# Kernel optimization log

Measured on AMD Instinct MI355X. Metric: run time of the kernel, lower is better.

Reference implementation:

```python
import jax, jax.numpy as jnp
import numpy as np

B, T, D, H = 4, 2048, 1024, 16
HD = D // H  # head_dim = 64


def setup_inputs() -> dict:
    key = jax.random.key(0)
    k1, k2, k3 = jax.random.split(key, 3)
    x = jax.random.normal(k1, (B, T, D), dtype=jnp.float32)
    # torch Linear weights: [out_features, in_features], kaiming-ish scale
    Wqkv = jax.random.normal(k2, (3 * D, D), dtype=jnp.float32) * (1.0 / np.sqrt(D))
    Wout = jax.random.normal(k3, (D, D), dtype=jnp.float32) * (1.0 / np.sqrt(D))
    return {"x": x, "Wqkv": Wqkv, "Wout": Wout}


def reference(x, Wqkv, Wout):
    b, t, c = x.shape
    qkv = x @ Wqkv.T                      # [B,T,3D]
    q, k, v = jnp.split(qkv, 3, axis=2)
    # [B,T,D] -> [B,H,T,HD]
    q = q.reshape(b, t, H, HD).transpose(0, 2, 1, 3)
    k = k.reshape(b, t, H, HD).transpose(0, 2, 1, 3)
    v = v.reshape(b, t, H, HD).transpose(0, 2, 1, 3)
    scale = 1.0 / np.sqrt(HD).astype(np.float32)
    att = jnp.einsum('bhqd,bhkd->bhqk', q, k) * scale  # [B,H,T,T]
    causal = jnp.tril(jnp.ones((t, t), dtype=bool))
    att = jnp.where(causal[None, None], att, -jnp.inf)
    att = jax.nn.softmax(att, axis=-1)
    y = jnp.einsum('bhqk,bhkd->bhqd', att, v)          # [B,H,T,HD]
    y = y.transpose(0, 2, 1, 3).reshape(b, t, c)       # [B,T,D]
    return y @ Wout.T
```

## Files before the change

kernel.cpp:

```cpp
#include <hip/hip_runtime.h>
#include <hip/hip_bf16.h>
#include <stdint.h>

#define B_ 4
#define T_ 2048
#define D_ 1024
#define H_ 16
#define M_ (B_*T_)
#define N1_ (3*D_)

typedef __attribute__((ext_vector_type(8))) short short8;
typedef __attribute__((ext_vector_type(4))) short short4v;
typedef __attribute__((ext_vector_type(4))) float f32x4;
typedef __attribute__((ext_vector_type(16))) float f32x16;

typedef const __attribute__((address_space(1))) void* as1cp;
typedef __attribute__((address_space(3))) void* as3p;

__device__ __forceinline__ ushort f2bf(float f) {
  union { float f; unsigned u; } v; v.f = f;
  unsigned r = v.u + 0x7fffu + ((v.u >> 16) & 1u);
  return (ushort)(r >> 16);
}

__device__ __forceinline__ float fast_exp2(float x) {
#if __has_builtin(__builtin_amdgcn_exp2f)
  return __builtin_amdgcn_exp2f(x);
#else
  float r;
  asm("v_exp_f32 %0, %1" : "=v"(r) : "v"(x));
  return r;
#endif
}

__global__ void cast3_f32_bf16(const float* __restrict__ a, ushort* __restrict__ oa, int na,
                               const float* __restrict__ b, ushort* __restrict__ ob, int nb,
                               const float* __restrict__ c, ushort* __restrict__ oc, int nc) {
  int i = blockIdx.x * blockDim.x + threadIdx.x;
  int stride = gridDim.x * blockDim.x;
  int ntot = na + nb + nc;
  for (; i < ntot; i += stride) {
    const float* src; ushort* dst; int j = i;
    if (j < na) { src = a; dst = oa; }
    else if ((j -= na) < nb) { src = b; dst = ob; }
    else { j -= nb; src = c; dst = oc; }
    float4 v = reinterpret_cast<const float4*>(src)[j];
    ushort4 o;
    o.x = f2bf(v.x); o.y = f2bf(v.y); o.z = f2bf(v.z); o.w = f2bf(v.w);
    reinterpret_cast<ushort4*>(dst)[j] = o;
  }
}

__device__ __forceinline__ void gload_lds16(const ushort* g, ushort* l) {
  __builtin_amdgcn_global_load_lds((as1cp)(const void*)g, (as3p)(void*)l, 16, 0, 0);
}

__device__ __forceinline__ short4v ds_tr16(unsigned addr) {
  short4v r;
  asm volatile("ds_read_b64_tr_b16 %0, %1" : "=v"(r) : "v"(addr) : "memory");
  return r;
}

__device__ __forceinline__ short8 cat8(short4v a, short4v b) {
  short8 r;
  r[0]=a[0]; r[1]=a[1]; r[2]=a[2]; r[3]=a[3];
  r[4]=b[0]; r[5]=b[1]; r[6]=b[2]; r[7]=b[3];
  return r;
}

__device__ __forceinline__ unsigned cvtpk(float lo, float hi) {
  unsigned r;
  asm("v_cvt_pk_bf16_f32 %0, %1, %2" : "=v"(r) : "v"(lo), "v"(hi));
  return r;
}

__device__ __forceinline__ f32x16 mfma32(short8 a, short8 b, f32x16 c) {
  return __builtin_amdgcn_mfma_f32_32x32x16_bf16(a, b, c, 0, 0, 0);
}

template<int MODE>
__global__ __launch_bounds__(256) void gemm_bt(const ushort* __restrict__ A,
                                               const ushort* __restrict__ Bm,
                                               void* __restrict__ Cout,
                                               int M, int N, int K, int gx) {
  __shared__ ushort Al[128*32];
  __shared__ ushort Bl[128*32];
  const int tid  = threadIdx.x;
  const int lane = tid & 63;
  const int w    = tid >> 6;
  const int g    = lane >> 4;
  const int ln   = lane & 15;

  const int nwg = gridDim.x;
  const int cpx = nwg >> 3;
  const int id  = (int)blockIdx.x;
  const int swz = (id & 7) * cpx + (id >> 3);
  const int m0 = (swz / gx) * 128;
  const int n0 = (swz % gx) * 128;
  const int wr = w >> 1, wc = w & 1;

  f32x4 acc[4][4] = {};

  for (int kt = 0; kt < K; kt += 32) {
    __syncthreads();
    #pragma unroll
    for (int j = 0; j < 2; ++j) {
      int cc  = w * 2 + j;
      int idx = cc * 64 + lane;
      int row = idx >> 2;
      int kofs = (idx & 3) * 8;
      gload_lds16(A  + (size_t)(m0 + row) * K + kt + kofs, &Al[cc * 512]);
      gload_lds16(Bm + (size_t)(n0 + row) * K + kt + kofs, &Bl[cc * 512]);
    }
    __syncthreads();
    short8 a[4], b[4];
    #pragma unroll
    for (int m = 0; m < 4; ++m)
      a[m] = *(const short8*)&Al[(wr*64 + m*16 + ln) * 32 + g*8];
    #pragma unroll
    for (int n = 0; n < 4; ++n)
      b[n] = *(const short8*)&Bl[(wc*64 + n*16 + ln) * 32 + g*8];
    #pragma unroll
    for (int m = 0; m < 4; ++m)
      #pragma unroll
      for (int n = 0; n < 4; ++n)
        acc[m][n] = __builtin_amdgcn_mfma_f32_16x16x32_bf16(a[m], b[n], acc[m][n], 0, 0, 0);
  }

  #pragma unroll
  for (int m = 0; m < 4; ++m) {
    int gr = m0 + wr*64 + m*16 + g*4;
    #pragma unroll
    for (int n = 0; n < 4; ++n) {
      int gc = n0 + wc*64 + n*16 + ln;
      #pragma unroll
      for (int r = 0; r < 4; ++r) {
        float v = acc[m][n][r];
        if (MODE == 2 && gc < 1024) v *= 0.18033688011112042f;
        if (MODE) ((ushort*)Cout)[(size_t)(gr + r) * N + gc] = f2bf(v);
        else      ((float*)Cout)[(size_t)(gr + r) * N + gc]  = v;
      }
    }
  }
}

__global__ __launch_bounds__(512, 2) void attn11(const ushort* __restrict__ qkv,
                                                 ushort* __restrict__ y) {
  __shared__ ushort Kl[2][8192];
  __shared__ ushort Vl[2][8192];

  const int tid  = threadIdx.x;
  const int lane = tid & 63;
  const int w    = tid >> 6;
  const int l31  = lane & 31;
  const int hi   = lane >> 5;

  const int bh = blockIdx.x;
  const int b  = bh >> 4;
  const int h  = bh & 15;
  const int qb = 7 - (int)blockIdx.y;
  const int rowg = b * T_;
  const int q0 = qb * 256;
  const int qw = q0 + w * 32;
  const int qrow = qw + l31;
  const int nt = 2 * qb + 2;

  const int krow0 = tid >> 3;
  const int kcb   = ((tid & 7) * 16) ^ ((krow0 & 7) << 4);
  const int vdh = tid & 1, vr = (tid >> 1) & 3, vg = (tid >> 3) & 3,
            vkq = (tid >> 5) & 1, vks = (tid >> 6) & 7;
  const int vkey = vks*16 + vkq*8 + (vg >> 1)*4 + vr;
  const int vdd  = (vg & 1)*16 + vdh*8;

  short8 qf[4];
  {
    const ushort* qp = qkv + (size_t)(rowg + qrow) * N1_ + h*64 + hi*8;
    #pragma unroll
    for (int kc = 0; kc < 4; ++kc) qf[kc] = *(const short8*)(qp + kc*16);
  }

  f32x16 oacc[2] = {};
  float lrun = 0.f;

  const unsigned VbBase = (unsigned)(size_t)(as3p)(void*)&Vl[0][0];
  const unsigned trln = (unsigned)(((lane >> 4) * 128) + (lane & 15) * 8);

  auto STAGE = [&](int bufi, int kb) {
    const ushort* Ks = qkv + (size_t)(rowg + kb + krow0) * N1_ + D_ + h*64 + (kcb >> 1);
    gload_lds16(Ks,                     &Kl[bufi][tid*8]);
    gload_lds16(Ks + (size_t)64 * N1_,  &Kl[bufi][(512 + tid)*8]);
    const ushort* Vs = qkv + (size_t)(rowg + kb + vkey) * N1_ + 2*D_ + h*64 + vdd;
    gload_lds16(Vs,      &Vl[bufi][tid*8]);
    gload_lds16(Vs + 32, &Vl[bufi][(512 + tid)*8]);
  };

  STAGE(0, 0);

  for (int kt = 0; kt < nt; ++kt) {
    const int buf = kt & 1;
    const int kbase = kt * 128;
    if (kt + 1 < nt) {
      STAGE(buf ^ 1, kbase + 128);
      asm volatile("s_waitcnt vmcnt(4)" ::: "memory");
    } else {
      asm volatile("s_waitcnt vmcnt(0)" ::: "memory");
    }
    asm volatile("s_barrier" ::: "memory");

    #pragma unroll
    for (int h2 = 0; h2 < 2; ++h2) {
      const int kb2 = kbase + h2 * 64;
      if (kb2 <= qw + 31) {
        f32x16 sv[2] = {};
        const char* Kb = (const char*)&Kl[buf][0] + h2 * 8192;
        __builtin_amdgcn_s_setprio(1);
        #pragma unroll
        for (int kc = 0; kc < 4; ++kc) {
          unsigned co = (unsigned)((kc*32 + hi*16) ^ ((l31 & 7) << 4));
          short8 k0 = *(const short8*)(Kb + (size_t)l31*128 + co);
          short8 k1 = *(const short8*)(Kb + (size_t)(32 + l31)*128 + co);
          sv[0] = mfma32(k0, qf[kc], sv[0]);
          sv[1] = mfma32(k1, qf[kc], sv[1]);
        }
        __builtin_amdgcn_s_setprio(0);

        if (kb2 + 63 > qw) {
          #pragma unroll
          for (int t = 0; t < 2; ++t)
            #pragma unroll
            for (int r = 0; r < 16; ++r) {
              int kl = kb2 + t*32 + (r & 3) + 8*(r >> 2) + 4*hi;
              if (kl > qrow) sv[t][r] = -1.0e38f;
            }
        }

        #pragma unroll
        for (int t = 0; t < 2; ++t)
          #pragma unroll
          for (int r = 0; r < 16; ++r) sv[t][r] = fast_exp2(sv[t][r]);
        float ts[8];
        #pragma unroll
        for (int r = 0; r < 8; ++r)
          ts[r] = (sv[0][r] + sv[0][r+8]) + (sv[1][r] + sv[1][r+8]);
        lrun += ((ts[0] + ts[1]) + (ts[2] + ts[3])) + ((ts[4] + ts[5]) + (ts[6] + ts[7]));

        const unsigned Vb = VbBase + (unsigned)(buf * 16384);
        short4v vt[2][4][2];
        #pragma unroll
        for (int dt = 0; dt < 2; ++dt)
          #pragma unroll
          for (int ks = 0; ks < 4; ++ks) {
            unsigned a = Vb + (unsigned)(dt*8192 + (h2*4 + ks)*1024) + trln;
            vt[dt][ks][0] = ds_tr16(a);
            vt[dt][ks][1] = ds_tr16(a + 512);
          }

        short8 pa[4];
        #pragma unroll
        for (int ks = 0; ks < 4; ++ks) {
          const int t = ks >> 1, base = 8 * (ks & 1);
          union { unsigned u[4]; short8 v; } uu;
          uu.u[0] = cvtpk(sv[t][base+0], sv[t][base+1]);
          uu.u[1] = cvtpk(sv[t][base+2], sv[t][base+3]);
          uu.u[2] = cvtpk(sv[t][base+4], sv[t][base+5]);
          uu.u[3] = cvtpk(sv[t][base+6], sv[t][base+7]);
          pa[ks] = uu.v;
        }

        asm volatile("s_waitcnt lgkmcnt(0)" ::: "memory");
        __builtin_amdgcn_sched_barrier(0);
        __builtin_amdgcn_s_setprio(1);
        #pragma unroll
        for (int ks = 0; ks < 4; ++ks) {
          oacc[0] = mfma32(cat8(vt[0][ks][0], vt[0][ks][1]), pa[ks], oacc[0]);
          oacc[1] = mfma32(cat8(vt[1][ks][0], vt[1][ks][1]), pa[ks], oacc[1]);
        }
        __builtin_amdgcn_s_setprio(0);
      }
    }
    asm volatile("s_barrier" ::: "memory");
  }

  float ltot = lrun + __shfl_xor(lrun, 32);
  const float inv = 1.0f / ltot;
  #pragma unroll
  for (int dt = 0; dt < 2; ++dt) {
    #pragma unroll
    for (int rq = 0; rq < 4; ++rq) {
      ushort4 pk4;
      pk4.x = f2bf(oacc[dt][rq*4+0] * inv);
      pk4.y = f2bf(oacc[dt][rq*4+1] * inv);
      pk4.z = f2bf(oacc[dt][rq*4+2] * inv);
      pk4.w = f2bf(oacc[dt][rq*4+3] * inv);
      *(ushort4*)&y[(size_t)(rowg + qrow) * D_ + h*64 + dt*32 + rq*8 + hi*4] = pk4;
    }
  }
}

extern "C" void kernel_launch(void* const* d_in, const int* in_sizes, int n_in,
                              void* d_out, int out_size, void* d_ws, size_t ws_size,
                              hipStream_t stream) {
  const float* x    = (const float*)d_in[0];
  const float* Wqkv = (const float*)d_in[1];
  const float* Wout = (const float*)d_in[2];

  ushort* xb    = (ushort*)d_ws;
  ushort* wqkvb = xb    + (size_t)M_ * D_;
  ushort* woutb = wqkvb + (size_t)N1_ * D_;
  ushort* qkvb  = woutb + (size_t)D_ * D_;
  ushort* yb    = qkvb  + (size_t)M_ * N1_;

  cast3_f32_bf16<<<2048, 256, 0, stream>>>(x, xb, M_ * D_ / 4,
                                           Wqkv, wqkvb, N1_ * D_ / 4,
                                           Wout, woutb, D_ * D_ / 4);

  gemm_bt<2><<<(N1_/128)*(M_/128), 256, 0, stream>>>(xb, wqkvb, qkvb, M_, N1_, D_, N1_/128);

  attn11<<<dim3(B_*H_, 8), 512, 0, stream>>>(qkvb, yb);

  gemm_bt<0><<<(D_/128)*(M_/128), 256, 0, stream>>>(yb, woutb, d_out, M_, D_, D_, D_/128);
}
```

Measured before the change: 167.8 us.

## Triple-buffer LDS tiles in GEMM with async prefetch and one barrier per step

Turns the bf16 GEMM main loop into a three-stage software pipeline. Global-to-LDS loads for tile t+2 are issued while tile t is consumed, and a vmcnt-based wait plus a single s_barrier replaces the two __syncthreads per K step. MFMA sections are also wrapped in s_setprio to favour matrix issue. The aim is to hide global memory latency behind compute, at the cost of three times the LDS footprint, which may lower occupancy.

```diff
diff --git a/kernel.cpp b/kernel.cpp
--- a/kernel.cpp
+++ b/kernel.cpp
@@ -79,12 +79,12 @@
 }
 
 template<int MODE>
-__global__ __launch_bounds__(256) void gemm_bt(const ushort* __restrict__ A,
+__global__ __launch_bounds__(256) void gemm_tb(const ushort* __restrict__ A,
                                                const ushort* __restrict__ Bm,
                                                void* __restrict__ Cout,
                                                int M, int N, int K, int gx) {
-  __shared__ ushort Al[128*32];
-  __shared__ ushort Bl[128*32];
+  __shared__ ushort Al[3][4096];
+  __shared__ ushort Bl[3][4096];
   const int tid  = threadIdx.x;
   const int lane = tid & 63;
   const int w    = tid >> 6;
@@ -99,32 +99,51 @@
   const int n0 = (swz % gx) * 128;
   const int wr = w >> 1, wc = w & 1;
 
+  int srow[2], skof[2], scc[2];
+  #pragma unroll
+  for (int j = 0; j < 2; ++j) {
+    int cc  = w * 2 + j;
+    int idx = cc * 64 + lane;
+    scc[j]  = cc;
+    srow[j] = idx >> 2;
+    skof[j] = (idx & 3) * 8;
+  }
+
+  auto STAGE = [&](int slot, int kt) {
+    #pragma unroll
+    for (int j = 0; j < 2; ++j) {
+      gload_lds16(A  + (size_t)(m0 + srow[j]) * K + kt + skof[j], &Al[slot][scc[j] * 512]);
+      gload_lds16(Bm + (size_t)(n0 + srow[j]) * K + kt + skof[j], &Bl[slot][scc[j] * 512]);
+    }
+  };
+
+  const int NT = K >> 5;
   f32x4 acc[4][4] = {};
 
-  for (int kt = 0; kt < K; kt += 32) {
-    __syncthreads();
-    #pragma unroll
-    for (int j = 0; j < 2; ++j) {
-      int cc  = w * 2 + j;
-      int idx = cc * 64 + lane;
-      int row = idx >> 2;
-      int kofs = (idx & 3) * 8;
-      gload_lds16(A  + (size_t)(m0 + row) * K + kt + kofs, &Al[cc * 512]);
-      gload_lds16(Bm + (size_t)(n0 + row) * K + kt + kofs, &Bl[cc * 512]);
-    }
-    __syncthreads();
+  STAGE(0, 0);
+  if (NT > 1) STAGE(1, 32);
+
+  for (int t = 0; t < NT; ++t) {
+    const int slot = t % 3;
+    if (t + 1 < NT) asm volatile("s_waitcnt vmcnt(4)" ::: "memory");
+    else            asm volatile("s_waitcnt vmcnt(0)" ::: "memory");
+    asm volatile("s_barrier" ::: "memory");
+    if (t + 2 < NT) STAGE((t + 2) % 3, (t + 2) * 32);
+
     short8 a[4], b[4];
     #pragma unroll
     for (int m = 0; m < 4; ++m)
-      a[m] = *(const short8*)&Al[(wr*64 + m*16 + ln) * 32 + g*8];
+      a[m] = *(const short8*)&Al[slot][(wr*64 + m*16 + ln) * 32 + g*8];
     #pragma unroll
     for (int n = 0; n < 4; ++n)
-      b[n] = *(const short8*)&Bl[(wc*64 + n*16 + ln) * 32 + g*8];
+      b[n] = *(const short8*)&Bl[slot][(wc*64 + n*16 + ln) * 32 + g*8];
+    __builtin_amdgcn_s_setprio(1);
     #pragma unroll
     for (int m = 0; m < 4; ++m)
       #pragma unroll
       for (int n = 0; n < 4; ++n)
         acc[m][n] = __builtin_amdgcn_mfma_f32_16x16x32_bf16(a[m], b[n], acc[m][n], 0, 0, 0);
+    __builtin_amdgcn_s_setprio(0);
   }
 
   #pragma unroll
@@ -314,9 +333,9 @@
                                            Wqkv, wqkvb, N1_ * D_ / 4,
                                            Wout, woutb, D_ * D_ / 4);
 
-  gemm_bt<2><<<(N1_/128)*(M_/128), 256, 0, stream>>>(xb, wqkvb, qkvb, M_, N1_, D_, N1_/128);
+  gemm_tb<2><<<(N1_/128)*(M_/128), 256, 0, stream>>>(xb, wqkvb, qkvb, M_, N1_, D_, N1_/128);
 
   attn11<<<dim3(B_*H_, 8), 512, 0, stream>>>(qkvb, yb);
 
-  gemm_bt<0><<<(D_/128)*(M_/128), 256, 0, stream>>>(yb, woutb, d_out, M_, D_, D_, D_/128);
-}
+  gemm_tb<0><<<(D_/128)*(M_/128), 256, 0, stream>>>(yb, woutb, d_out, M_, D_, D_, D_/128);
+}
```

Result: faster. 160.4 us (-4.4%).
